# Performance work log

Measured on AMD Instinct MI355X. Metric: run time of the kernel, lower is better.

## Reference

```python
import jax, jax.numpy as jnp
import numpy as np

B, T, F_IN, F_OUT = 16, 2048, 128, 128
ALPHA = 0.2  # LeakyReLU negative slope
MASK_VAL = -1e9


def setup_inputs() -> dict:
    key = jax.random.key(0)
    kx, kw, ka, kadj = jax.random.split(key, 4)
    # xavier_uniform-ish scale for W and a (gain=1.414)
    w_bound = 1.414 * np.sqrt(6.0 / (F_IN + F_OUT))
    a_bound = 1.414 * np.sqrt(6.0 / (2 * F_OUT + 1))
    x = jax.random.normal(kx, (B, T, F_IN), jnp.float32)
    W = jax.random.uniform(kw, (F_IN, F_OUT), jnp.float32, -w_bound, w_bound)
    a = jax.random.uniform(ka, (2 * F_OUT, 1), jnp.float32, -a_bound, a_bound)
    adj = jax.random.randint(kadj, (B, T, T), 0, 2, jnp.int32)
    return {"x": x, "adj": adj, "W": W, "a": a}


def reference(x, adj, W, a):
    # h: [B,T,F_OUT]
    h = jnp.einsum('btf,fo->bto', x, W)
    # Additive GAT score decomposition: e[b,i,j] = leakyrelu(h_i . a1 + h_j . a2)
    # Mathematically identical to cat([h_i,h_j]) @ a, without the BxTxTx2F tensor.
    a1 = a[:F_OUT, 0]   # [F_OUT]
    a2 = a[F_OUT:, 0]   # [F_OUT]
    s1 = h @ a1         # [B,T]
    s2 = h @ a2         # [B,T]
    e = jax.nn.leaky_relu(s1[:, :, None] + s2[:, None, :], ALPHA)  # [B,T,T]
    e = jnp.where(adj == 0, MASK_VAL, e)
    att = jax.nn.softmax(e, axis=-1)  # [B,T,T]
    # dropout=0.0 / eval mode -> identity
    return att @ h  # [B,T,F_OUT]
```

## Files before the change

kernel.cpp:

```cpp
#include <hip/hip_runtime.h>
#include <hip/hip_bf16.h>

#define TT 2048
#define NB 16
#define FD 128
#define ALPHA 0.2f

typedef __attribute__((ext_vector_type(8))) short short8;
typedef __attribute__((ext_vector_type(4))) float f32x4;
typedef __attribute__((ext_vector_type(16))) float f32x16;

static __device__ __forceinline__ unsigned short f2bf(float f) {
    unsigned u = __float_as_uint(f);
    u += 0x7FFF + ((u >> 16) & 1);
    return (unsigned short)(u >> 16);
}
static __device__ __forceinline__ unsigned short bfbits(float f) {
    return __builtin_bit_cast(unsigned short, __float2bfloat16(f));
}

__global__ __launch_bounds__(256) void k_wt(const float* __restrict__ W,
                                            unsigned short* __restrict__ WT)
{
    int fid = blockIdx.x * 256 + threadIdx.x;
    int k = fid >> 5;
    int f = (fid & 31) << 2;
    float4 w4 = *reinterpret_cast<const float4*>(W + k * FD + f);
    WT[(f + 0) * FD + k] = f2bf(w4.x);
    WT[(f + 1) * FD + k] = f2bf(w4.y);
    WT[(f + 2) * FD + k] = f2bf(w4.z);
    WT[(f + 3) * FD + k] = f2bf(w4.w);
}

__global__ __launch_bounds__(256) void k_h(const float* __restrict__ x,
                                           const unsigned short* __restrict__ WT,
                                           const float* __restrict__ a,
                                           unsigned short* __restrict__ hF,
                                           float* __restrict__ s1,
                                           float* __restrict__ s2)
{
    __shared__ unsigned short hs[128][72];

    const int tid = threadIdx.x;
    const int b  = blockIdx.x >> 5;
    const int t0 = (blockIdx.x & 31) << 6;
    const int w = tid >> 6, l = tid & 63, g = l >> 4, r15 = l & 15;

    const float* xrow = x + ((size_t)(b * TT + t0 + w * 16 + r15)) * FD;

    f32x4 acc[8] = {};

    #pragma unroll
    for (int m = 0; m < 4; ++m) {
        const int koff = m * 32 + g * 8;
        float4 xa = *reinterpret_cast<const float4*>(xrow + koff);
        float4 xb = *reinterpret_cast<const float4*>(xrow + koff + 4);
        short8 af;
        af[0] = (short)f2bf(xa.x); af[1] = (short)f2bf(xa.y);
        af[2] = (short)f2bf(xa.z); af[3] = (short)f2bf(xa.w);
        af[4] = (short)f2bf(xb.x); af[5] = (short)f2bf(xb.y);
        af[6] = (short)f2bf(xb.z); af[7] = (short)f2bf(xb.w);
        #pragma unroll
        for (int n = 0; n < 8; ++n) {
            short8 bfr = *reinterpret_cast<const short8*>(WT + (n * 16 + r15) * FD + koff);
            acc[n] = __builtin_amdgcn_mfma_f32_16x16x32_bf16(af, bfr, acc[n], 0, 0, 0);
        }
    }

    float p1[4] = {0.f, 0.f, 0.f, 0.f}, p2[4] = {0.f, 0.f, 0.f, 0.f};
    #pragma unroll
    for (int n = 0; n < 8; ++n) {
        float a1v = a[n * 16 + r15];
        float a2v = a[FD + n * 16 + r15];
        #pragma unroll
        for (int r = 0; r < 4; ++r) {
            p1[r] += acc[n][r] * a1v;
            p2[r] += acc[n][r] * a2v;
        }
    }
    #pragma unroll
    for (int r = 0; r < 4; ++r) {
        #pragma unroll
        for (int off = 8; off >= 1; off >>= 1) {
            p1[r] += __shfl_xor(p1[r], off);
            p2[r] += __shfl_xor(p2[r], off);
        }
    }
    if (r15 == 0) {
        const int trow = t0 + w * 16 + g * 4;
        #pragma unroll
        for (int r = 0; r < 4; ++r) {
            s1[b * TT + trow + r] = p1[r];
            s2[b * TT + trow + r] = p2[r];
        }
    }

    #pragma unroll
    for (int n = 0; n < 8; ++n)
        #pragma unroll
        for (int r = 0; r < 4; ++r)
            hs[n * 16 + r15][w * 16 + g * 4 + r] = f2bf(acc[n][r]);
    __syncthreads();

    #pragma unroll
    for (int it = 0; it < 4; ++it) {
        int idx = it * 256 + tid;
        int lp = idx & 63;
        int frag = idx >> 6;
        int n32 = frag & 3, tl = frag >> 2;
        int fsrc = n32 * 32 + (lp & 31);
        int tsrc = tl * 16 + (lp >> 5) * 8;
        short8 v = *reinterpret_cast<const short8*>(&hs[fsrc][tsrc]);
        *reinterpret_cast<short8*>(
            hF + (((size_t)(b * 128 + (t0 >> 4) + tl)) * 4 + n32) * 512 + lp * 8) = v;
    }
}

__global__ __launch_bounds__(256, 3) void k_att(const int* __restrict__ adj,
                                                const unsigned short* __restrict__ hF,
                                                const float* __restrict__ s1,
                                                const float* __restrict__ s2,
                                                float* __restrict__ out)
{
    __shared__ __align__(16) float red[2][32][132];
    __shared__ float dsum[4][32];

    const int tid = threadIdx.x;
    const int wg = (blockIdx.x & 7) * 128 + (blockIdx.x >> 3);
    const int b  = wg >> 6;
    const int i0 = (wg & 63) << 5;
    const int w = tid >> 6, l = tid & 63;
    const int il = l & 31, h = l >> 5;

    const int jbeg = w * (TT / 4);
    const float s1v = s1[b * TT + i0 + il];
    const float* s2p = s2 + b * TT + jbeg + h * 8;
    const int* adjp = adj + ((size_t)(b * TT + i0 + il)) * TT + jbeg + h * 8;
    const unsigned short* hfp = hF + ((size_t)(b * 128 + (jbeg >> 4))) * 4 * 512 + l * 8;

    f32x16 acc[4] = {};
    float rsum = 0.f;

    short8 bb[2][4];
    #pragma unroll
    for (int n = 0; n < 4; ++n)
        bb[0][n] = *reinterpret_cast<const short8*>(hfp + (size_t)n * 512);

    int4 ar[2][2];
    ar[0][0] = *reinterpret_cast<const int4*>(adjp);
    ar[0][1] = *reinterpret_cast<const int4*>(adjp + 4);

    #pragma unroll
    for (int t = 0; t < 32; ++t) {
        const int cur = t & 1;
        if (t < 31) {
            ar[cur ^ 1][0] = *reinterpret_cast<const int4*>(adjp + (t + 1) * 16);
            ar[cur ^ 1][1] = *reinterpret_cast<const int4*>(adjp + (t + 1) * 16 + 4);
            #pragma unroll
            for (int n = 0; n < 4; ++n)
                bb[cur ^ 1][n] = *reinterpret_cast<const short8*>(
                    hfp + (size_t)((t + 1) * 4 + n) * 512);
        }

        float4 sa = *reinterpret_cast<const float4*>(s2p + t * 16);
        float4 sb = *reinterpret_cast<const float4*>(s2p + t * 16 + 4);
        float csf[8] = {sa.x, sa.y, sa.z, sa.w, sb.x, sb.y, sb.z, sb.w};
        const int ad[8] = {ar[cur][0].x, ar[cur][0].y, ar[cur][0].z, ar[cur][0].w,
                           ar[cur][1].x, ar[cur][1].y, ar[cur][1].z, ar[cur][1].w};
        float pv[8];
        #pragma unroll
        for (int e = 0; e < 8; ++e) {
            float s = s1v + csf[e];
            s = fmaxf(s, ALPHA * s);
            float p = ad[e] ? __expf(s) : 0.f;
            rsum += p;
            pv[e] = p;
        }
        short8 af;
        #pragma unroll
        for (int e = 0; e < 8; ++e)
            af[e] = (short)bfbits(pv[e]);
        #pragma unroll
        for (int n = 0; n < 4; ++n)
            acc[n] = __builtin_amdgcn_mfma_f32_32x32x16_bf16(af, bb[cur][n], acc[n], 0, 0, 0);
    }

    rsum += __shfl_xor(rsum, 32);
    if (l < 32) dsum[w][l] = rsum;

    if (w < 2) {
        #pragma unroll
        for (int n = 0; n < 4; ++n)
            #pragma unroll
            for (int r = 0; r < 16; ++r) {
                int irow = (r & 3) + 8 * (r >> 2) + 4 * h;
                red[w][irow][n * 32 + il] = acc[n][r];
            }
    }
    __syncthreads();
    if (w >= 2) {
        #pragma unroll
        for (int n = 0; n < 4; ++n)
            #pragma unroll
            for (int r = 0; r < 16; ++r) {
                int irow = (r & 3) + 8 * (r >> 2) + 4 * h;
                red[w - 2][irow][n * 32 + il] += acc[n][r];
            }
    }
    __syncthreads();

    #pragma unroll
    for (int it = 0; it < 4; ++it) {
        int e = it * 256 + tid;
        int row = e >> 5;
        int c4 = (e & 31) << 2;
        float4 v0 = *reinterpret_cast<const float4*>(&red[0][row][c4]);
        float4 v1 = *reinterpret_cast<const float4*>(&red[1][row][c4]);
        float dn = dsum[0][row] + dsum[1][row] + dsum[2][row] + dsum[3][row];
        float ri = 1.0f / dn;
        float4 o;
        o.x = (v0.x + v1.x) * ri;
        o.y = (v0.y + v1.y) * ri;
        o.z = (v0.z + v1.z) * ri;
        o.w = (v0.w + v1.w) * ri;
        *reinterpret_cast<float4*>(out + ((size_t)(b * TT + i0 + row)) * FD + c4) = o;
    }
}

extern "C" void kernel_launch(void* const* d_in, const int* in_sizes, int n_in,
                              void* d_out, int out_size, void* d_ws, size_t ws_size,
                              hipStream_t stream)
{
    const float* x  = (const float*)d_in[0];
    const int* adj  = (const int*)d_in[1];
    const float* W  = (const float*)d_in[2];
    const float* a  = (const float*)d_in[3];
    float* out = (float*)d_out;

    unsigned short* hF = (unsigned short*)d_ws;
    float* s1 = (float*)((char*)d_ws + (size_t)NB * FD * TT * 2);
    float* s2 = s1 + NB * TT;
    unsigned short* WT = (unsigned short*)(s2 + NB * TT);

    k_wt <<<16, 256, 0, stream>>>(W, WT);
    k_h  <<<NB * (TT / 64), 256, 0, stream>>>(x, WT, a, hF, s1, s2);
    k_att<<<NB * (TT / 32), 256, 0, stream>>>(adj, hF, s1, s2, out);
}
```

Baseline: 117.3 us.

## Coalesce adjacency loads via ballot bitmasks and stage s2 in LDS

The adjacency matrix is now read with lanes spanning consecutive columns, so each row load is coalesced. Each row is turned into a bitmask with ballot and byte-permute, then routed to the owning lane and used to gate the exponentials. The s2 scores are staged once per block in shared memory, and hF fragments are prefetched four steps at a time per 64-column chunk. The price is many more live registers (two 32-int staging arrays plus 16 B fragments), so occupancy is lowered from 3 to 2 blocks per SIMD, along with extra ballot and select work.

```diff
diff --git a/kernel.cpp b/kernel.cpp
--- a/kernel.cpp
+++ b/kernel.cpp
@@ -116,12 +116,13 @@
     }
 }
 
-__global__ __launch_bounds__(256, 3) void k_att(const int* __restrict__ adj,
+__global__ __launch_bounds__(256, 2) void k_att(const int* __restrict__ adj,
                                                 const unsigned short* __restrict__ hF,
                                                 const float* __restrict__ s1,
                                                 const float* __restrict__ s2,
                                                 float* __restrict__ out)
 {
+    __shared__ float s2b[TT];
     __shared__ __align__(16) float red[2][32][132];
     __shared__ float dsum[4][32];
 
@@ -132,57 +133,81 @@
     const int w = tid >> 6, l = tid & 63;
     const int il = l & 31, h = l >> 5;
 
+    {
+        float4 v0 = *reinterpret_cast<const float4*>(s2 + b * TT + tid * 8);
+        float4 v1 = *reinterpret_cast<const float4*>(s2 + b * TT + tid * 8 + 4);
+        *reinterpret_cast<float4*>(&s2b[tid * 8])     = v0;
+        *reinterpret_cast<float4*>(&s2b[tid * 8 + 4]) = v1;
+    }
+    const float s1v = s1[b * TT + i0 + il];
+    __syncthreads();
+
     const int jbeg = w * (TT / 4);
-    const float s1v = s1[b * TT + i0 + il];
-    const float* s2p = s2 + b * TT + jbeg + h * 8;
-    const int* adjp = adj + ((size_t)(b * TT + i0 + il)) * TT + jbeg + h * 8;
+    const int* aw = adj + ((size_t)(b * TT + i0)) * TT + jbeg + l;
     const unsigned short* hfp = hF + ((size_t)(b * 128 + (jbeg >> 4))) * 4 * 512 + l * 8;
+    const unsigned selH = h ? 0x07050301u : 0x06040200u;
+    const float* s2w = &s2b[jbeg + h * 8];
 
     f32x16 acc[4] = {};
     float rsum = 0.f;
 
-    short8 bb[2][4];
-    #pragma unroll
-    for (int n = 0; n < 4; ++n)
-        bb[0][n] = *reinterpret_cast<const short8*>(hfp + (size_t)n * 512);
-
-    int4 ar[2][2];
-    ar[0][0] = *reinterpret_cast<const int4*>(adjp);
-    ar[0][1] = *reinterpret_cast<const int4*>(adjp + 4);
-
-    #pragma unroll
-    for (int t = 0; t < 32; ++t) {
-        const int cur = t & 1;
-        if (t < 31) {
-            ar[cur ^ 1][0] = *reinterpret_cast<const int4*>(adjp + (t + 1) * 16);
-            ar[cur ^ 1][1] = *reinterpret_cast<const int4*>(adjp + (t + 1) * 16 + 4);
+    int sA[32], sB[32];
+    #pragma unroll
+    for (int r = 0; r < 32; ++r)
+        sA[r] = aw[(size_t)r * TT];
+
+    auto chunk = [&](const int c, int (&stC)[32], int (&stN)[32]) {
+        short8 bbC[4][4];
+        #pragma unroll
+        for (int s = 0; s < 4; ++s)
             #pragma unroll
             for (int n = 0; n < 4; ++n)
-                bb[cur ^ 1][n] = *reinterpret_cast<const short8*>(
-                    hfp + (size_t)((t + 1) * 4 + n) * 512);
-        }
-
-        float4 sa = *reinterpret_cast<const float4*>(s2p + t * 16);
-        float4 sb = *reinterpret_cast<const float4*>(s2p + t * 16 + 4);
-        float csf[8] = {sa.x, sa.y, sa.z, sa.w, sb.x, sb.y, sb.z, sb.w};
-        const int ad[8] = {ar[cur][0].x, ar[cur][0].y, ar[cur][0].z, ar[cur][0].w,
-                           ar[cur][1].x, ar[cur][1].y, ar[cur][1].z, ar[cur][1].w};
-        float pv[8];
-        #pragma unroll
-        for (int e = 0; e < 8; ++e) {
-            float s = s1v + csf[e];
-            s = fmaxf(s, ALPHA * s);
-            float p = ad[e] ? __expf(s) : 0.f;
-            rsum += p;
-            pv[e] = p;
-        }
-        short8 af;
-        #pragma unroll
-        for (int e = 0; e < 8; ++e)
-            af[e] = (short)bfbits(pv[e]);
-        #pragma unroll
-        for (int n = 0; n < 4; ++n)
-            acc[n] = __builtin_amdgcn_mfma_f32_32x32x16_bf16(af, bb[cur][n], acc[n], 0, 0, 0);
+                bbC[s][n] = *reinterpret_cast<const short8*>(
+                    hfp + (size_t)((c * 4 + s) * 4 + n) * 512);
+        if (c < 7) {
+            #pragma unroll
+            for (int r = 0; r < 32; ++r)
+                stN[r] = aw[(size_t)r * TT + (c + 1) * 64];
+        }
+        unsigned bits = 0;
+        #pragma unroll
+        for (int r = 0; r < 32; ++r) {
+            unsigned long long m = __ballot(stC[r] != 0);
+            unsigned pm = __builtin_amdgcn_perm((unsigned)(m >> 32),
+                                                (unsigned)m, selH);
+            bits = (il == r) ? pm : bits;
+        }
+        #pragma unroll
+        for (int s = 0; s < 4; ++s) {
+            const int T = c * 4 + s;
+            const unsigned bt = (bits >> (s * 8)) & 0xffu;
+            float4 sa = *reinterpret_cast<const float4*>(&s2w[T * 16]);
+            float4 sb = *reinterpret_cast<const float4*>(&s2w[T * 16 + 4]);
+            float csf[8] = {sa.x, sa.y, sa.z, sa.w, sb.x, sb.y, sb.z, sb.w};
+            float pv[8];
+            #pragma unroll
+            for (int e = 0; e < 8; ++e) {
+                float sc = s1v + csf[e];
+                sc = fmaxf(sc, ALPHA * sc);
+                float p = ((int)(bt << (31 - e)) < 0) ? __expf(sc) : 0.f;
+                rsum += p;
+                pv[e] = p;
+            }
+            short8 af;
+            #pragma unroll
+            for (int e = 0; e < 8; ++e)
+                af[e] = (short)bfbits(pv[e]);
+            #pragma unroll
+            for (int n = 0; n < 4; ++n)
+                acc[n] = __builtin_amdgcn_mfma_f32_32x32x16_bf16(af, bbC[s][n],
+                                                                 acc[n], 0, 0, 0);
+        }
+    };
+
+    #pragma unroll
+    for (int cc = 0; cc < 4; ++cc) {
+        chunk(2 * cc,     sA, sB);
+        chunk(2 * cc + 1, sB, sA);
     }
 
     rsum += __shfl_xor(rsum, 32);
```

After: 180.6 us. 1.54x slower.
